# Kernel optimization log

Hardware: AMD Instinct MI355X
Metric: run time of the kernel (lower is better)

## Reference

```python
import jax, jax.numpy as jnp
import numpy as np

B, CIN, COUT, N, H, W = 8, 64, 64, 16, 32, 32

def cell_centered_grid(h, w):
    # (h, w, h, w, 4) cell-centered coords in [0,1], then mapped to [-1,1]
    dims = (h, w, h, w)
    axes = [(jnp.arange(d, dtype=jnp.float32) + 0.5) / d for d in dims]
    mesh = jnp.meshgrid(*axes, indexing='ij')
    coords = jnp.stack(mesh, axis=-1)
    return 2.0 * coords - 1.0

def setup_inputs() -> dict:
    key = jax.random.key(0)
    ks = jax.random.split(key, 9)
    v = jax.random.normal(ks[0], (B, CIN, H, W), dtype=jnp.float32)
    params = jax.random.normal(ks[1], (N, COUT, CIN), dtype=jnp.float32) / np.sqrt(N * CIN)
    # coeff_mlp: Linear(4,8) -> GELU -> Linear(8,N), torch default init
    w1 = jax.random.uniform(ks[2], (8, 4), jnp.float32, -1/np.sqrt(4), 1/np.sqrt(4))
    b1 = jax.random.uniform(ks[3], (8,), jnp.float32, -1/np.sqrt(4), 1/np.sqrt(4))
    w2 = jax.random.uniform(ks[4], (N, 8), jnp.float32, -1/np.sqrt(8), 1/np.sqrt(8))
    b2 = jax.random.uniform(ks[5], (N,), jnp.float32, -1/np.sqrt(8), 1/np.sqrt(8))
    # 1x1 conv
    cstd = 1/np.sqrt(CIN)
    conv_w = jax.random.uniform(ks[6], (COUT, CIN), jnp.float32, -cstd, cstd)
    conv_b = jax.random.uniform(ks[7], (COUT,), jnp.float32, -cstd, cstd)
    bias = jax.random.uniform(ks[8], (COUT, 1, 1), jnp.float32, -cstd, cstd)
    return {"v": v, "params": params, "w1": w1, "b1": b1, "w2": w2, "b2": b2,
            "conv_w": conv_w, "conv_b": conv_b, "bias": bias}

def reference(v, params, w1, b1, w2, b2, conv_w, conv_b, bias):
    h, w = v.shape[-2], v.shape[-1]
    coords = cell_centered_grid(h, w)                       # (h1,w1,h2,w2,4)
    hid = jax.nn.gelu(coords @ w1.T + b1, approximate=False)
    coeffs = hid @ w2.T + b2                                # (h1,w1,h2,w2,n)
    # contract coeffs with v over input spatial dims first (small intermediate)
    tmp = jnp.einsum('xyhwn,bixy->bnihw', coeffs, v)        # (B,n,i,h2,w2)
    t = jnp.einsum('bnihw,noi->bohw', tmp, params) / (h * w)
    conv = jnp.einsum('bihw,oi->bohw', v, conv_w) + conv_b[None, :, None, None]
    out = t + conv + bias[None]
    return out
```

## Files before the change

### kernel.cpp

```cpp
#include <hip/hip_runtime.h>
#include <hip/hip_bf16.h>
#include <math.h>

#define WSB_LTAB  0u
#define WSB_QM    262144u
#define WSB_RB2   393216u
#define WSB_WPART 409600u
#define WSB_VSUMP 2506752u

#define COS8_INIT {0.98078528f, 0.83146961f, 0.55557023f, 0.19509032f, \
                  -0.19509032f, -0.55557023f, -0.83146961f, -0.98078528f}

__device__ inline float gelu_exact(float z) {
    return 0.5f * z * (1.0f + erff(z * 0.70710678118f));
}

__device__ inline float cheb_hwid(const float* w1, int c) {
    return fmaxf((fabsf(w1[c * 4 + 2]) + fabsf(w1[c * 4 + 3])) * (31.0f / 32.0f), 1e-2f);
}

__global__ __launch_bounds__(256) void wgemm_kernel(const float* __restrict__ v,
                                                    const float* __restrict__ params,
                                                    const float* __restrict__ w1,
                                                    const float* __restrict__ b1,
                                                    const float* __restrict__ w2,
                                                    const float* __restrict__ b2,
                                                    char* __restrict__ wsb) {
    const float COS8[8] = COS8_INIT;
    float* Ltab  = (float*)(wsb + WSB_LTAB);
    float* Qm    = (float*)(wsb + WSB_QM);
    float* Rb2   = (float*)(wsb + WSB_RB2);
    float* Wpart = (float*)(wsb + WSB_WPART);
    float* VsumP = (float*)(wsb + WSB_VSUMP);
    __shared__ float Vs[16][68];
    __shared__ float Gs[64][64];
    int t = threadIdx.x;
    int bi0 = blockIdx.x * 16, xy0 = blockIdx.y * 64;
    {
        int r = t >> 4, c4 = t & 15;
        *(float4*)&Vs[r][c4 * 4] = *(const float4*)(v + (bi0 + r) * 1024 + xy0 + c4 * 4);
    }
    #pragma unroll
    for (int l = 0; l < 16; l++) {
        int e = t + l * 256;
        int xyl = e >> 6, cr = e & 63, c = cr >> 3, r = cr & 7;
        int xy = xy0 + xyl;
        float cx = 2.0f * (((xy >> 5) + 0.5f) / 32.0f) - 1.0f;
        float cy = 2.0f * (((xy & 31) + 0.5f) / 32.0f) - 1.0f;
        float z = cx * w1[c * 4 + 0] + cy * w1[c * 4 + 1] + b1[c]
                + cheb_hwid(w1, c) * COS8[r];
        Gs[xyl][cr] = gelu_exact(z);
    }
    __syncthreads();
    int bl = t >> 4, crq = t & 15;
    float4 acc = make_float4(0.f, 0.f, 0.f, 0.f);
    float vs = 0.0f;
    #pragma unroll 8
    for (int xy = 0; xy < 64; xy++) {
        float a = Vs[bl][xy];
        float4 g = *(const float4*)&Gs[xy][crq * 4];
        acc.x += a * g.x; acc.y += a * g.y; acc.z += a * g.z; acc.w += a * g.w;
        vs += a;
    }
    *(float4*)(Wpart + (size_t)blockIdx.y * 32768 + (bi0 + bl) * 64 + crq * 4) = acc;
    if (crq == 0) VsumP[blockIdx.y * 512 + bi0 + bl] = vs;

    int bid = blockIdx.y * 32 + blockIdx.x;
    int u = bid * 200 + t;
    if (t < 200) {
        if (u < 65536) {
            int cr = u >> 10, hw = u & 1023, c = cr >> 3, r = cr & 7;
            float hwid = cheb_hwid(w1, c);
            float ch = 2.0f * (((hw >> 5) + 0.5f) / 32.0f) - 1.0f;
            float cw = 2.0f * (((hw & 31) + 0.5f) / 32.0f) - 1.0f;
            float vv = ch * w1[c * 4 + 2] + cw * w1[c * 4 + 3];
            float tr = hwid * COS8[r];
            float p = 1.0f, d = 1.0f;
            #pragma unroll
            for (int s = 0; s < 8; s++)
                if (s != r) {
                    float ts = hwid * COS8[s];
                    p *= (vv - ts);
                    d *= (tr - ts);
                }
            Ltab[u] = p / d;
        } else if (u < 98304) {
            int u2 = u - 65536;
            int c = u2 >> 12, oi = u2 & 4095;
            float s = 0.0f;
            #pragma unroll
            for (int n = 0; n < 16; n++)
                s += params[n * 4096 + oi] * w2[n * 8 + c];
            Qm[u2] = s * (1.0f / 1024.0f);
        } else {
            int oi = u - 98304;
            float s = 0.0f;
            #pragma unroll
            for (int n = 0; n < 16; n++)
                s += params[n * 4096 + oi] * b2[n];
            Rb2[oi] = s * (1.0f / 1024.0f);
        }
    }
}

__global__ __launch_bounds__(256) void final_kernel(const float* __restrict__ v,
                                                    const float* __restrict__ conv_w,
                                                    const float* __restrict__ conv_b,
                                                    const float* __restrict__ bias,
                                                    float* __restrict__ out,
                                                    char* __restrict__ wsb) {
    const float* Ltab  = (const float*)(wsb + WSB_LTAB);
    const float* Qm    = (const float*)(wsb + WSB_QM);
    const float* Rb2   = (const float*)(wsb + WSB_RB2);
    const float* Wpart = (const float*)(wsb + WSB_WPART);
    const float* VsumP = (const float*)(wsb + WSB_VSUMP);
    __shared__ float smem[128 * 36 + 128 * 64];
    __shared__ float Esh[32];
    __shared__ float Vsh[64];
    float* Ct = smem;
    float* Ys = smem + 128 * 36;
    float* Wsum = Ys;
    int t = threadIdx.x;
    int hw0 = blockIdx.x * 64, o0 = blockIdx.y * 32, b = blockIdx.z;

    {
        int e0 = t * 16;
        float4 a0 = {0,0,0,0}, a1 = {0,0,0,0}, a2 = {0,0,0,0}, a3 = {0,0,0,0};
        const float* wp = Wpart + b * 4096 + e0;
        #pragma unroll
        for (int ks = 0; ks < 16; ks++) {
            const float4* p = (const float4*)(wp + (size_t)ks * 32768);
            float4 x0 = p[0], x1 = p[1], x2 = p[2], x3 = p[3];
            a0.x += x0.x; a0.y += x0.y; a0.z += x0.z; a0.w += x0.w;
            a1.x += x1.x; a1.y += x1.y; a1.z += x1.z; a1.w += x1.w;
            a2.x += x2.x; a2.y += x2.y; a2.z += x2.z; a2.w += x2.w;
            a3.x += x3.x; a3.y += x3.y; a3.z += x3.z; a3.w += x3.w;
        }
        *(float4*)&Wsum[e0]      = a0;
        *(float4*)&Wsum[e0 + 4]  = a1;
        *(float4*)&Wsum[e0 + 8]  = a2;
        *(float4*)&Wsum[e0 + 12] = a3;
    }
    if (t < 64) {
        float s = 0.0f;
        #pragma unroll
        for (int ks = 0; ks < 16; ks++) s += VsumP[ks * 512 + b * 64 + t];
        Vsh[t] = s;
    }
    #pragma unroll
    for (int l = 0; l < 8; l++) {
        int e = t + l * 256;
        int kk = e >> 5, ol = e & 31;
        Ct[(64 + kk) * 36 + ol] = conv_w[(o0 + ol) * 64 + kk];
    }
    #pragma unroll
    for (int l = 0; l < 4; l++) {
        int f = t + l * 256;
        int k = f >> 4, q = f & 15;
        *(float4*)&Ys[(64 + k) * 64 + q * 4] =
            *(const float4*)(v + (size_t)b * 65536 + k * 1024 + hw0 + q * 4);
    }
    __syncthreads();

    {
        int ol = t >> 3, c = t & 7;
        float a[8] = {};
        const float* qrow = Qm + c * 4096 + (o0 + ol) * 64;
        for (int i = 0; i < 64; i++) {
            float q = qrow[i];
            float4 w0 = *(const float4*)&Wsum[i * 64 + c * 8];
            float4 w1v = *(const float4*)&Wsum[i * 64 + c * 8 + 4];
            a[0] += q * w0.x; a[1] += q * w0.y; a[2] += q * w0.z; a[3] += q * w0.w;
            a[4] += q * w1v.x; a[5] += q * w1v.y; a[6] += q * w1v.z; a[7] += q * w1v.w;
        }
        #pragma unroll
        for (int r = 0; r < 8; r++)
            Ct[(c * 8 + r) * 36 + ol] = a[r];
    }
    if (t < 32) {
        int o = o0 + t;
        float s = conv_b[o] + bias[o];
        const float* rr = Rb2 + o * 64;
        for (int i = 0; i < 64; i++) s += rr[i] * Vsh[i];
        Esh[t] = s;
    }
    __syncthreads();

    #pragma unroll
    for (int l = 0; l < 4; l++) {
        int f = t + l * 256;
        int k = f >> 4, q = f & 15;
        *(float4*)&Ys[k * 64 + q * 4] =
            *(const float4*)(Ltab + (size_t)k * 1024 + hw0 + q * 4);
    }
    __syncthreads();

    int ty = t >> 5, tx = t & 31;
    float acc[4][2];
    #pragma unroll
    for (int m = 0; m < 4; m++) {
        float e = Esh[ty * 4 + m];
        acc[m][0] = e; acc[m][1] = e;
    }
    #pragma unroll 4
    for (int k = 0; k < 128; k++) {
        float4 cq = *(const float4*)&Ct[k * 36 + ty * 4];
        float2 y = *(const float2*)&Ys[k * 64 + tx * 2];
        acc[0][0] += cq.x * y.x; acc[0][1] += cq.x * y.y;
        acc[1][0] += cq.y * y.x; acc[1][1] += cq.y * y.y;
        acc[2][0] += cq.z * y.x; acc[2][1] += cq.z * y.y;
        acc[3][0] += cq.w * y.x; acc[3][1] += cq.w * y.y;
    }
    #pragma unroll
    for (int m = 0; m < 4; m++) {
        float2 r = make_float2(acc[m][0], acc[m][1]);
        *(float2*)(out + (size_t)b * 65536 + (o0 + ty * 4 + m) * 1024 + hw0 + tx * 2) = r;
    }
}

extern "C" void kernel_launch(void* const* d_in, const int* in_sizes, int n_in,
                              void* d_out, int out_size, void* d_ws, size_t ws_size,
                              hipStream_t stream) {
    const float* v      = (const float*)d_in[0];
    const float* params = (const float*)d_in[1];
    const float* w1     = (const float*)d_in[2];
    const float* b1     = (const float*)d_in[3];
    const float* w2     = (const float*)d_in[4];
    const float* b2     = (const float*)d_in[5];
    const float* conv_w = (const float*)d_in[6];
    const float* conv_b = (const float*)d_in[7];
    const float* bias   = (const float*)d_in[8];
    float* out = (float*)d_out;
    char* wsb  = (char*)d_ws;

    wgemm_kernel<<<dim3(32, 16), 256, 0, stream>>>(v, params, w1, b1, w2, b2, wsb);
    final_kernel<<<dim3(16, 2, 8), 256, 0, stream>>>(v, conv_w, conv_b, bias, out, wsb);
}
```

Measured before the change: 93.51 us.

## Double final_kernel threads with split-K reduction and separate Wsum buffer

The final kernel now launches 512 threads per block instead of 256. Each phase's work (Wpart reduction, Ct computation, tile loads) is split across twice as many threads. The main 128-deep K loop is split into two halves whose partials are reduced through shared memory. Wsum gets its own shared buffer, so the Ltab tile load can be issued in the first load phase instead of after an extra barrier. This costs more shared memory and one extra reduction barrier, in exchange for more latency hiding with only 256 blocks on the grid.

```diff
diff --git a/kernel.cpp b/kernel.cpp
--- a/kernel.cpp
+++ b/kernel.cpp
@@ -103,7 +103,7 @@
     }
 }
 
-__global__ __launch_bounds__(256) void final_kernel(const float* __restrict__ v,
+__global__ __launch_bounds__(512) void final_kernel(const float* __restrict__ v,
                                                     const float* __restrict__ conv_w,
                                                     const float* __restrict__ conv_b,
                                                     const float* __restrict__ bias,
@@ -114,32 +114,28 @@
     const float* Rb2   = (const float*)(wsb + WSB_RB2);
     const float* Wpart = (const float*)(wsb + WSB_WPART);
     const float* VsumP = (const float*)(wsb + WSB_VSUMP);
-    __shared__ float smem[128 * 36 + 128 * 64];
+    __shared__ float Ct[128 * 36];
+    __shared__ float Ys[128 * 64];
+    __shared__ float Ws[64 * 64];
     __shared__ float Esh[32];
     __shared__ float Vsh[64];
-    float* Ct = smem;
-    float* Ys = smem + 128 * 36;
-    float* Wsum = Ys;
     int t = threadIdx.x;
     int hw0 = blockIdx.x * 64, o0 = blockIdx.y * 32, b = blockIdx.z;
 
     {
-        int e0 = t * 16;
-        float4 a0 = {0,0,0,0}, a1 = {0,0,0,0}, a2 = {0,0,0,0}, a3 = {0,0,0,0};
+        int e0 = t * 8;
+        float4 a0 = make_float4(0.f, 0.f, 0.f, 0.f);
+        float4 a1 = make_float4(0.f, 0.f, 0.f, 0.f);
         const float* wp = Wpart + b * 4096 + e0;
         #pragma unroll
         for (int ks = 0; ks < 16; ks++) {
             const float4* p = (const float4*)(wp + (size_t)ks * 32768);
-            float4 x0 = p[0], x1 = p[1], x2 = p[2], x3 = p[3];
+            float4 x0 = p[0], x1 = p[1];
             a0.x += x0.x; a0.y += x0.y; a0.z += x0.z; a0.w += x0.w;
             a1.x += x1.x; a1.y += x1.y; a1.z += x1.z; a1.w += x1.w;
-            a2.x += x2.x; a2.y += x2.y; a2.z += x2.z; a2.w += x2.w;
-            a3.x += x3.x; a3.y += x3.y; a3.z += x3.z; a3.w += x3.w;
-        }
-        *(float4*)&Wsum[e0]      = a0;
-        *(float4*)&Wsum[e0 + 4]  = a1;
-        *(float4*)&Wsum[e0 + 8]  = a2;
-        *(float4*)&Wsum[e0 + 12] = a3;
+        }
+        *(float4*)&Ws[e0]     = a0;
+        *(float4*)&Ws[e0 + 4] = a1;
     }
     if (t < 64) {
         float s = 0.0f;
@@ -148,34 +144,39 @@
         Vsh[t] = s;
     }
     #pragma unroll
-    for (int l = 0; l < 8; l++) {
-        int e = t + l * 256;
+    for (int l = 0; l < 4; l++) {
+        int e = t + l * 512;
         int kk = e >> 5, ol = e & 31;
         Ct[(64 + kk) * 36 + ol] = conv_w[(o0 + ol) * 64 + kk];
     }
     #pragma unroll
-    for (int l = 0; l < 4; l++) {
-        int f = t + l * 256;
+    for (int l = 0; l < 2; l++) {
+        int f = t + l * 512;
         int k = f >> 4, q = f & 15;
         *(float4*)&Ys[(64 + k) * 64 + q * 4] =
             *(const float4*)(v + (size_t)b * 65536 + k * 1024 + hw0 + q * 4);
     }
+    #pragma unroll
+    for (int l = 0; l < 2; l++) {
+        int f = t + l * 512;
+        int k = f >> 4, q = f & 15;
+        *(float4*)&Ys[k * 64 + q * 4] =
+            *(const float4*)(Ltab + (size_t)k * 1024 + hw0 + q * 4);
+    }
     __syncthreads();
 
     {
-        int ol = t >> 3, c = t & 7;
-        float a[8] = {};
+        int ol = t >> 4, c = (t >> 1) & 7, hi = t & 1;
+        float a[4] = {};
         const float* qrow = Qm + c * 4096 + (o0 + ol) * 64;
         for (int i = 0; i < 64; i++) {
             float q = qrow[i];
-            float4 w0 = *(const float4*)&Wsum[i * 64 + c * 8];
-            float4 w1v = *(const float4*)&Wsum[i * 64 + c * 8 + 4];
-            a[0] += q * w0.x; a[1] += q * w0.y; a[2] += q * w0.z; a[3] += q * w0.w;
-            a[4] += q * w1v.x; a[5] += q * w1v.y; a[6] += q * w1v.z; a[7] += q * w1v.w;
-        }
-        #pragma unroll
-        for (int r = 0; r < 8; r++)
-            Ct[(c * 8 + r) * 36 + ol] = a[r];
+            float4 w = *(const float4*)&Ws[i * 64 + c * 8 + hi * 4];
+            a[0] += q * w.x; a[1] += q * w.y; a[2] += q * w.z; a[3] += q * w.w;
+        }
+        #pragma unroll
+        for (int j = 0; j < 4; j++)
+            Ct[(c * 8 + hi * 4 + j) * 36 + ol] = a[j];
     }
     if (t < 32) {
         int o = o0 + t;
@@ -186,35 +187,39 @@
     }
     __syncthreads();
 
-    #pragma unroll
-    for (int l = 0; l < 4; l++) {
-        int f = t + l * 256;
-        int k = f >> 4, q = f & 15;
-        *(float4*)&Ys[k * 64 + q * 4] =
-            *(const float4*)(Ltab + (size_t)k * 1024 + hw0 + q * 4);
-    }
-    __syncthreads();
-
-    int ty = t >> 5, tx = t & 31;
+    int g = t >> 8, tt = t & 255;
+    int ty = tt >> 5, tx = tt & 31;
     float acc[4][2];
     #pragma unroll
     for (int m = 0; m < 4; m++) {
-        float e = Esh[ty * 4 + m];
+        float e = (g == 0) ? Esh[ty * 4 + m] : 0.0f;
         acc[m][0] = e; acc[m][1] = e;
     }
     #pragma unroll 4
-    for (int k = 0; k < 128; k++) {
-        float4 cq = *(const float4*)&Ct[k * 36 + ty * 4];
-        float2 y = *(const float2*)&Ys[k * 64 + tx * 2];
+    for (int k = 0; k < 64; k++) {
+        int kk = g * 64 + k;
+        float4 cq = *(const float4*)&Ct[kk * 36 + ty * 4];
+        float2 y = *(const float2*)&Ys[kk * 64 + tx * 2];
         acc[0][0] += cq.x * y.x; acc[0][1] += cq.x * y.y;
         acc[1][0] += cq.y * y.x; acc[1][1] += cq.y * y.y;
         acc[2][0] += cq.z * y.x; acc[2][1] += cq.z * y.y;
         acc[3][0] += cq.w * y.x; acc[3][1] += cq.w * y.y;
     }
-    #pragma unroll
-    for (int m = 0; m < 4; m++) {
-        float2 r = make_float2(acc[m][0], acc[m][1]);
-        *(float2*)(out + (size_t)b * 65536 + (o0 + ty * 4 + m) * 1024 + hw0 + tx * 2) = r;
+    if (g == 1) {
+        *(float4*)&Ws[tt * 8]     = make_float4(acc[0][0], acc[0][1], acc[1][0], acc[1][1]);
+        *(float4*)&Ws[tt * 8 + 4] = make_float4(acc[2][0], acc[2][1], acc[3][0], acc[3][1]);
+    }
+    __syncthreads();
+    if (g == 0) {
+        float4 p0 = *(const float4*)&Ws[tt * 8];
+        float4 p1 = *(const float4*)&Ws[tt * 8 + 4];
+        acc[0][0] += p0.x; acc[0][1] += p0.y; acc[1][0] += p0.z; acc[1][1] += p0.w;
+        acc[2][0] += p1.x; acc[2][1] += p1.y; acc[3][0] += p1.z; acc[3][1] += p1.w;
+        #pragma unroll
+        for (int m = 0; m < 4; m++) {
+            *(float2*)(out + (size_t)b * 65536 + (o0 + ty * 4 + m) * 1024 + hw0 + tx * 2)
+                = make_float2(acc[m][0], acc[m][1]);
+        }
     }
 }
 
@@ -234,5 +239,5 @@
     char* wsb  = (char*)d_ws;
 
     wgemm_kernel<<<dim3(32, 16), 256, 0, stream>>>(v, params, w1, b1, w2, b2, wsb);
-    final_kernel<<<dim3(16, 2, 8), 256, 0, stream>>>(v, conv_w, conv_b, bias, out, wsb);
-}
+    final_kernel<<<dim3(16, 2, 8), 512, 0, stream>>>(v, conv_w, conv_b, bias, out, wsb);
+}
```

Result: faster. 88.57 us (median of 2 runs) (-5.3%).
